# Kernel tuning notes

Hardware: AMD Instinct MI355X
Metric: run time of the kernel (lower is better)

The kernel has to match this reference:

```python
import jax, jax.numpy as jnp
import numpy as np

B, INPUT, MEM, CELL, HEADS, K = 32, 512, 32768, 64, 1, 16
VIS = K + 1  # visible_size = sparse_reads + 1


def setup_inputs() -> dict:
    key = jax.random.key(0)
    ks = jax.random.split(key, 8)
    n = lambda k, s: jax.random.normal(k, s, jnp.float32)
    scale = 0.05  # small init so tanh/sigmoid stay in useful range
    return {
        "xi": n(ks[0], (B, INPUT)),
        "memory": n(ks[1], (B, MEM, CELL)),
        "least_used_mem": jax.random.randint(ks[2], (B, 1), 0, MEM),
        "W_rq": n(ks[3], (HEADS * CELL, INPUT)) * scale,
        "b_rq": jnp.zeros((HEADS * CELL,), jnp.float32),
        "W_wv": n(ks[4], (CELL, INPUT)) * scale,
        "b_wv": jnp.zeros((CELL,), jnp.float32),
        "W_ig": n(ks[5], (VIS, INPUT)) * scale,
        "b_ig": jnp.zeros((VIS,), jnp.float32),
        "W_wg": n(ks[6], (1, INPUT)) * scale,
        "b_wg": jnp.zeros((1,), jnp.float32),
    }


def reference(xi, memory, least_used_mem, W_rq, b_rq, W_wv, b_wv, W_ig, b_ig, W_wg, b_wg):
    b = xi.shape[0]
    # interface transforms (independent_linears=True path)
    read_query = jnp.tanh(xi @ W_rq.T + b_rq).reshape(b, HEADS, CELL)
    write_vector = jnp.tanh(xi @ W_wv.T + b_wv).reshape(b, 1, CELL)
    interpolation_gate = jax.nn.sigmoid(xi @ W_ig.T + b_ig)          # [b, VIS]
    write_gate = jax.nn.sigmoid(xi @ W_wg.T + b_wg)                  # [b, 1]

    # kNN search over memory (torch.topk fallback path of read_from_sparse_memory)
    sims = jnp.einsum("bhc,bmc->bhm", read_query, memory)            # [b, H, MEM]
    _, idx = jax.lax.top_k(sims, K)                                  # [b, H, K]
    read_positions = jnp.concatenate([idx.reshape(b, -1), least_used_mem], axis=1)  # [b, VIS]

    # gather visible memory cells
    visible_memory = jnp.take_along_axis(memory, read_positions[:, :, None], axis=1)  # [b, VIS, CELL]

    # attention over visible cells
    rw = jax.nn.softmax(jnp.einsum("bhc,bvc->bhv", read_query, visible_memory), axis=2)  # [b, H, VIS]
    read_vectors = jnp.einsum("bhv,bvc->bhc", rw, visible_memory)    # [b, H, CELL]
    rw_flat = rw.sum(axis=1)                                         # [b, VIS]

    # scatter read weights into full memory-sized vector (torch scatter_ = set)
    read_weights = jnp.zeros((b, MEM), xi.dtype).at[
        jnp.arange(b)[:, None], read_positions
    ].set(rw_flat)                                                   # [b, MEM]

    return read_vectors, read_weights, visible_memory, write_vector, interpolation_gate, write_gate
```

## Files before the change

kernel.cpp:

```cpp
#include <hip/hip_runtime.h>
#include <cstdint>
#include <cstddef>
#include <cfloat>
#include <cmath>

#define NB    32
#define NIN   512
#define NMEM  32768
#define NCELL 64
#define NVIS  17
#define NK    16
#define NBLK  32
#define RPB   (NMEM / NBLK)
#define NCAND (NBLK * NK)

#define OFF_RV  0
#define OFF_RW  2048
#define OFF_VIS 1050624
#define OFF_WV  1085440
#define OFF_IG  1087488
#define OFF_WG  1088032

#define SCR_RQ  0
#define SCR_CV  64
#define SCR_CI  576
#define SCR_STRIDE_WS 1088

__global__ __launch_bounds__(256) void kA(
    const float* __restrict__ xi,
    const float* __restrict__ Wrq, const float* __restrict__ brq,
    const float* __restrict__ Wwv, const float* __restrict__ bwv,
    const float* __restrict__ Wig, const float* __restrict__ big,
    const float* __restrict__ Wwg, const float* __restrict__ bwg,
    float* __restrict__ scr_base, int scr_stride,
    float* __restrict__ out)
{
    int b = blockIdx.x;
    int tid = threadIdx.x;
    float* rq_scr = scr_base + (size_t)b * scr_stride + SCR_RQ;
    __shared__ float sxi[NIN];
    for (int i = tid; i < NIN; i += 256)
        sxi[i] = xi[(size_t)b * NIN + i];
    __syncthreads();
    int g = tid >> 3, sub = tid & 7;
    int row = blockIdx.y * 32 + g;
    if (row < 146) {
        const float* W; float bias; int kind, r;
        if (row < 64)       { r = row;       W = Wrq + (size_t)r * NIN; bias = brq[r]; kind = 0; }
        else if (row < 128) { r = row - 64;  W = Wwv + (size_t)r * NIN; bias = bwv[r]; kind = 1; }
        else if (row < 145) { r = row - 128; W = Wig + (size_t)r * NIN; bias = big[r]; kind = 2; }
        else                { r = 0;         W = Wwg;                   bias = bwg[0]; kind = 3; }
        float acc = 0.f;
        const float* wp = W   + sub * 64;
        const float* xp = sxi + sub * 64;
        for (int j = 0; j < 64; ++j)
            acc = fmaf(wp[j], xp[j], acc);
        acc += __shfl_xor(acc, 1);
        acc += __shfl_xor(acc, 2);
        acc += __shfl_xor(acc, 4);
        if (sub == 0) {
            float x = acc + bias;
            if (kind == 0)      rq_scr[r] = tanhf(x);
            else if (kind == 1) out[OFF_WV + b * NCELL + r] = tanhf(x);
            else if (kind == 2) out[OFF_IG + b * NVIS + r]  = 1.f / (1.f + expf(-x));
            else                out[OFF_WG + b]             = 1.f / (1.f + expf(-x));
        }
    }
}

__global__ __launch_bounds__(256) void kB(
    const float* __restrict__ mem,
    float* __restrict__ scr_base, int scr_stride, int kb_zero,
    float* __restrict__ out)
{
    int b   = blockIdx.y;
    int blk = blockIdx.x;
    int tid = threadIdx.x;
    int w = tid >> 6, lane = tid & 63;
    int cs = lane & 15;
    int rg = lane >> 4;
    float* scr = scr_base + (size_t)b * scr_stride;
    __shared__ float part[4][64 * 17];
    __shared__ float ssim[4][256];
    __shared__ float wcv[64];
    __shared__ int   wci[64];

    if (kb_zero) {
        float4 z; z.x = z.y = z.z = z.w = 0.f;
        ((float4*)(out + OFF_RW + (size_t)b * NMEM + blk * RPB))[tid] = z;
    }

    float rq4[4];
    for (int e = 0; e < 4; ++e) rq4[e] = scr[SCR_RQ + cs * 4 + e];

    const float* mb = mem + (size_t)b * NMEM * NCELL + (size_t)(blk * RPB + w * 256) * NCELL;

    for (int p = 0; p < 4; ++p) {
        #pragma unroll
        for (int it = 0; it < 4; ++it) {
            const float* base = mb + (size_t)(p * 64 + it * 16 + rg) * NCELL + cs * 4;
            float4 x0 = *(const float4*)(base);
            float4 x1 = *(const float4*)(base + 4 * NCELL);
            float4 x2 = *(const float4*)(base + 8 * NCELL);
            float4 x3 = *(const float4*)(base + 12 * NCELL);
            float p0 = fmaf(x0.w, rq4[3], fmaf(x0.z, rq4[2], fmaf(x0.y, rq4[1], x0.x * rq4[0])));
            float p1 = fmaf(x1.w, rq4[3], fmaf(x1.z, rq4[2], fmaf(x1.y, rq4[1], x1.x * rq4[0])));
            float p2 = fmaf(x2.w, rq4[3], fmaf(x2.z, rq4[2], fmaf(x2.y, rq4[1], x2.x * rq4[0])));
            float p3 = fmaf(x3.w, rq4[3], fmaf(x3.z, rq4[2], fmaf(x3.y, rq4[1], x3.x * rq4[0])));
            part[w][(it * 16 +  0 + rg) * 17 + cs] = p0;
            part[w][(it * 16 +  4 + rg) * 17 + cs] = p1;
            part[w][(it * 16 +  8 + rg) * 17 + cs] = p2;
            part[w][(it * 16 + 12 + rg) * 17 + cs] = p3;
        }
        __syncthreads();

        float s = 0.f;
        #pragma unroll
        for (int k = 0; k < 16; ++k)
            s += part[w][lane * 17 + k];
        ssim[w][p * 64 + lane] = s;
        __syncthreads();
    }

    int gbase = blk * RPB + w * 256;
    float v[4]; int gi[4];
    for (int j = 0; j < 4; ++j) {
        v[j]  = ssim[w][lane * 4 + j];
        gi[j] = gbase + lane * 4 + j;
    }
    for (int r = 0; r < NK; ++r) {
        float bv = v[0]; int bi = gi[0];
        for (int j = 1; j < 4; ++j)
            if (v[j] > bv || (v[j] == bv && gi[j] < bi)) { bv = v[j]; bi = gi[j]; }
        for (int off = 32; off >= 1; off >>= 1) {
            float ov = __shfl_xor(bv, off); int oi = __shfl_xor(bi, off);
            if (ov > bv || (ov == bv && oi < bi)) { bv = ov; bi = oi; }
        }
        for (int j = 0; j < 4; ++j)
            if (gi[j] == bi) { v[j] = -FLT_MAX; gi[j] = 0x7fffffff; }
        if (lane == 0) { wcv[w * 16 + r] = bv; wci[w * 16 + r] = bi; }
    }
    __syncthreads();

    if (w == 0) {
        float mv2 = wcv[lane]; int mi2 = wci[lane];
        float* ovp = scr + SCR_CV + blk * NK;
        int*   oip = (int*)(scr + SCR_CI) + blk * NK;
        for (int r = 0; r < NK; ++r) {
            float bv = mv2; int bi = mi2;
            for (int off = 32; off >= 1; off >>= 1) {
                float ov = __shfl_xor(bv, off); int oi = __shfl_xor(bi, off);
                if (ov > bv || (ov == bv && oi < bi)) { bv = ov; bi = oi; }
            }
            if (mi2 == bi) { mv2 = -FLT_MAX; mi2 = 0x7fffffff; }
            if (lane == 0) { ovp[r] = bv; oip[r] = bi; }
        }
    }
}

__global__ __launch_bounds__(256) void kC(
    const float* __restrict__ mem, const int* __restrict__ lum,
    const float* __restrict__ scr_base, int scr_stride, int kc_zero,
    float* __restrict__ out)
{
    int b = blockIdx.x;
    int tid = threadIdx.x;
    int w = tid >> 6, lane = tid & 63;
    float* rwrow = out + OFF_RW + (size_t)b * NMEM;
    const float* scr = scr_base + (size_t)b * scr_stride;
    __shared__ float lv[NCAND];
    __shared__ int   li[NCAND];
    __shared__ int   pos_s[NVIS];
    __shared__ float sc_s[NVIS];
    __shared__ float rw_s[NVIS];
    __shared__ float pacc[4][NCELL];

    for (int j = 0; j < 2; ++j) {
        int e = tid * 2 + j;
        lv[e] = scr[SCR_CV + e];
        li[e] = ((const int*)(scr + SCR_CI))[e];
    }
    __syncthreads();

    if (w == 0) {
        float v[8]; int gi[8];
        for (int j = 0; j < 8; ++j) { v[j] = lv[lane * 8 + j]; gi[j] = li[lane * 8 + j]; }
        for (int r = 0; r < NK; ++r) {
            float bv = v[0]; int bi = gi[0];
            for (int j = 1; j < 8; ++j)
                if (v[j] > bv || (v[j] == bv && gi[j] < bi)) { bv = v[j]; bi = gi[j]; }
            for (int off = 32; off >= 1; off >>= 1) {
                float ov = __shfl_xor(bv, off); int oi = __shfl_xor(bi, off);
                if (ov > bv || (ov == bv && oi < bi)) { bv = ov; bi = oi; }
            }
            for (int j = 0; j < 8; ++j)
                if (gi[j] == bi) { v[j] = -FLT_MAX; gi[j] = 0x7fffffff; }
            if (lane == 0) { pos_s[r] = bi & (NMEM - 1); sc_s[r] = bv; }
        }
        int p16 = lum[b] & (NMEM - 1);
        float x = mem[((size_t)b * NMEM + p16) * NCELL + lane] * scr[SCR_RQ + lane];
        for (int off = 32; off >= 1; off >>= 1) x += __shfl_xor(x, off);
        if (lane == 0) { pos_s[NK] = p16; sc_s[NK] = x; }
    }
    __syncthreads();

    if (w == 0) {
        float sc = (lane < NVIS) ? sc_s[lane] : -FLT_MAX;
        float mx = sc;
        for (int off = 32; off >= 1; off >>= 1) mx = fmaxf(mx, __shfl_xor(mx, off));
        float e = (lane < NVIS) ? expf(sc - mx) : 0.f;
        float sum = e;
        for (int off = 32; off >= 1; off >>= 1) sum += __shfl_xor(sum, off);
        if (lane < NVIS) rw_s[lane] = e / sum;
    }
    __syncthreads();

    if (kc_zero) {
        for (int it = 0; it < 128; ++it)
            rwrow[it * 256 + tid] = 0.f;
    }

    float acc = 0.f;
    for (int vv = w; vv < NVIS; vv += 4) {
        int p = pos_s[vv] & (NMEM - 1);
        float hv = mem[((size_t)b * NMEM + p) * NCELL + lane];
        out[OFF_VIS + ((size_t)b * NVIS + vv) * NCELL + lane] = hv;
        acc = fmaf(rw_s[vv], hv, acc);
    }
    pacc[w][lane] = acc;
    __syncthreads();

    if (tid < NCELL) {
        float s = pacc[0][tid] + pacc[1][tid] + pacc[2][tid] + pacc[3][tid];
        out[OFF_RV + b * NCELL + tid] = s;
    }
    if (tid < NVIS) {
        int p = pos_s[tid] & (NMEM - 1);
        bool dup = (tid < NK) && (p == pos_s[NK]);
        if (!dup) rwrow[p] = rw_s[tid];
    }
}

extern "C" void kernel_launch(void* const* d_in, const int* in_sizes, int n_in,
                              void* d_out, int out_size, void* d_ws, size_t ws_size,
                              hipStream_t stream)
{
    const float* xi  = (const float*)d_in[0];
    const float* mem = (const float*)d_in[1];
    const int*   lum = (const int*)d_in[2];
    const float* Wrq = (const float*)d_in[3];
    const float* brq = (const float*)d_in[4];
    const float* Wwv = (const float*)d_in[5];
    const float* bwv = (const float*)d_in[6];
    const float* Wig = (const float*)d_in[7];
    const float* big = (const float*)d_in[8];
    const float* Wwg = (const float*)d_in[9];
    const float* bwg = (const float*)d_in[10];
    float* out = (float*)d_out;

    bool use_ws = (d_ws != nullptr) && (ws_size >= (size_t)NB * SCR_STRIDE_WS * 4);
    float* scrb = use_ws ? (float*)d_ws : out + OFF_RW;
    int    scrs = use_ws ? SCR_STRIDE_WS : NMEM;
    int    kb_zero = use_ws ? 1 : 0;
    int    kc_zero = use_ws ? 0 : 1;

    kA<<<dim3(NB, 5), dim3(256), 0, stream>>>(xi, Wrq, brq, Wwv, bwv, Wig, big,
                                              Wwg, bwg, scrb, scrs, out);
    kB<<<dim3(NBLK, NB), dim3(256), 0, stream>>>(mem, scrb, scrs, kb_zero, out);
    kC<<<dim3(NB), dim3(256), 0, stream>>>(mem, lum, scrb, scrs, kc_zero, out);
}
```

Measured before the change: 90.68 us.

## Double-buffer memory rows into LDS via async global_load_lds and shuffle-reduce dots

Each wave now streams its 256 memory rows in 16-row tiles straight into LDS with global_load_lds, double-buffering the next tile while the current one is used for the dot products. The per-row partial dot products are reduced with xor shuffles instead of being written to a padded LDS array and summed, which removes the block-wide barriers inside the loop. The intent is to overlap global loads with compute and cut LDS traffic and synchronisation. The risk is that the hand-placed vmcnt waits and the sched barriers are fragile, and the mapping from lanes to rows changes.

```diff
diff --git a/kernel.cpp b/kernel.cpp
--- a/kernel.cpp
+++ b/kernel.cpp
@@ -25,6 +25,12 @@
 #define SCR_CV  64
 #define SCR_CI  576
 #define SCR_STRIDE_WS 1088
+
+__device__ __forceinline__ void gld16(const float* g, float* l) {
+    __builtin_amdgcn_global_load_lds(
+        (const __attribute__((address_space(1))) unsigned int*)g,
+        (__attribute__((address_space(3))) unsigned int*)l, 16, 0, 0);
+}
 
 __global__ __launch_bounds__(256) void kA(
     const float* __restrict__ xi,
@@ -80,7 +86,7 @@
     int cs = lane & 15;
     int rg = lane >> 4;
     float* scr = scr_base + (size_t)b * scr_stride;
-    __shared__ float part[4][64 * 17];
+    __shared__ __align__(16) float buf[4][2][16 * 64];
     __shared__ float ssim[4][256];
     __shared__ float wcv[64];
     __shared__ int   wci[64];
@@ -92,35 +98,50 @@
 
     float rq4[4];
     for (int e = 0; e < 4; ++e) rq4[e] = scr[SCR_RQ + cs * 4 + e];
+    asm volatile("" : "+v"(rq4[0]), "+v"(rq4[1]), "+v"(rq4[2]), "+v"(rq4[3]));
+    asm volatile("s_waitcnt vmcnt(0)" ::: "memory");
+    __builtin_amdgcn_sched_barrier(0);
 
     const float* mb = mem + (size_t)b * NMEM * NCELL + (size_t)(blk * RPB + w * 256) * NCELL;
-
-    for (int p = 0; p < 4; ++p) {
+    float* buf0 = &buf[w][0][0];
+    float* buf1 = &buf[w][1][0];
+
+    #pragma unroll
+    for (int i = 0; i < 4; ++i)
+        gld16(mb + i * 256 + lane * 4, buf0 + i * 256);
+
+    for (int t = 0; t < 16; ++t) {
+        float* cur = (t & 1) ? buf1 : buf0;
+        float* nxt = (t & 1) ? buf0 : buf1;
+        if (t < 15) {
+            const float* gt = mb + (size_t)(t + 1) * 1024;
+            #pragma unroll
+            for (int i = 0; i < 4; ++i)
+                gld16(gt + i * 256 + lane * 4, nxt + i * 256);
+            asm volatile("s_waitcnt vmcnt(4)" ::: "memory");
+        } else {
+            asm volatile("s_waitcnt vmcnt(0)" ::: "memory");
+        }
+        __builtin_amdgcn_sched_barrier(0);
+
+        float r[4];
         #pragma unroll
-        for (int it = 0; it < 4; ++it) {
-            const float* base = mb + (size_t)(p * 64 + it * 16 + rg) * NCELL + cs * 4;
-            float4 x0 = *(const float4*)(base);
-            float4 x1 = *(const float4*)(base + 4 * NCELL);
-            float4 x2 = *(const float4*)(base + 8 * NCELL);
-            float4 x3 = *(const float4*)(base + 12 * NCELL);
-            float p0 = fmaf(x0.w, rq4[3], fmaf(x0.z, rq4[2], fmaf(x0.y, rq4[1], x0.x * rq4[0])));
-            float p1 = fmaf(x1.w, rq4[3], fmaf(x1.z, rq4[2], fmaf(x1.y, rq4[1], x1.x * rq4[0])));
-            float p2 = fmaf(x2.w, rq4[3], fmaf(x2.z, rq4[2], fmaf(x2.y, rq4[1], x2.x * rq4[0])));
-            float p3 = fmaf(x3.w, rq4[3], fmaf(x3.z, rq4[2], fmaf(x3.y, rq4[1], x3.x * rq4[0])));
-            part[w][(it * 16 +  0 + rg) * 17 + cs] = p0;
-            part[w][(it * 16 +  4 + rg) * 17 + cs] = p1;
-            part[w][(it * 16 +  8 + rg) * 17 + cs] = p2;
-            part[w][(it * 16 + 12 + rg) * 17 + cs] = p3;
-        }
-        __syncthreads();
-
-        float s = 0.f;
-        #pragma unroll
-        for (int k = 0; k < 16; ++k)
-            s += part[w][lane * 17 + k];
-        ssim[w][p * 64 + lane] = s;
-        __syncthreads();
-    }
+        for (int j = 0; j < 4; ++j) {
+            float4 x = *(const float4*)(cur + lane * 4 + j * 256);
+            float p = fmaf(x.w, rq4[3], fmaf(x.z, rq4[2], fmaf(x.y, rq4[1], x.x * rq4[0])));
+            p += __shfl_xor(p, 1);
+            p += __shfl_xor(p, 2);
+            p += __shfl_xor(p, 4);
+            p += __shfl_xor(p, 8);
+            r[j] = p;
+        }
+        if (cs == 0) {
+            #pragma unroll
+            for (int j = 0; j < 4; ++j)
+                ssim[w][t * 16 + rg + 4 * j] = r[j];
+        }
+    }
+    __syncthreads();
 
     int gbase = blk * RPB + w * 256;
     float v[4]; int gi[4];
```

Result: slower. 93.72 us (+3.3%).
